# Performance work log

Measured on AMD Instinct MI355X. Metric: run time of the kernel, lower is better.

The kernel has to match this reference:

```python
import jax, jax.numpy as jnp
import numpy as np

H = 16      # headNum
C = 64      # cDim
D = 1024    # qDim = kDim = vDim = outDim
N = 2       # batch
S = 1024    # seq len


def setup_inputs() -> dict:
    key = jax.random.key(0)
    ks = jax.random.split(key, 12)
    inp = {
        "Qin": jax.random.normal(ks[0], (N, S, D), dtype=jnp.float32),
        "Kin": jax.random.normal(ks[1], (N, S, D), dtype=jnp.float32),
        "Vin": jax.random.normal(ks[2], (N, S, D), dtype=jnp.float32),
        "seqMask": jax.random.randint(ks[3], (N, S), 0, 2).astype(jnp.bool_),
        "attMask": jax.random.normal(ks[4], (1, 1, S, S), dtype=jnp.float32),
        # learned parameters (stored as [in, out] for x @ W)
        "QTrans": jax.random.normal(ks[5], (D, H * C), dtype=jnp.float32) * 0.02,
        "KTrans": jax.random.normal(ks[6], (D, H * C), dtype=jnp.float32) * 0.02,
        "VTrans": jax.random.normal(ks[7], (D, H * C), dtype=jnp.float32) * 0.02,
        "GTrans_w": jax.random.normal(ks[8], (D, H * C), dtype=jnp.float32) * 0.02,
        "GTrans_b": jnp.ones((H * C,), dtype=jnp.float32),
        "out_w": jax.random.normal(ks[9], (H * C, D), dtype=jnp.float32) * 0.02,
        "out_b": jnp.zeros((D,), dtype=jnp.float32),
    }
    return inp


def _split_heads(x):
    # [n, s, h*c] -> [h, n, s, c]
    n, s, _ = x.shape
    return x.reshape(n, s, H, C).transpose(2, 0, 1, 3)


def reference(Qin, Kin, Vin, seqMask, attMask, QTrans, KTrans, VTrans,
              GTrans_w, GTrans_b, out_w, out_b):
    Q = _split_heads(Qin @ QTrans)                         # [h,n,s,c]
    K = _split_heads(Kin @ KTrans)                         # [h,n,t,c]
    V = _split_heads(Vin @ VTrans)                         # [h,n,t,c]
    G = jax.nn.sigmoid(_split_heads(Vin @ GTrans_w + GTrans_b))  # [h,n,s,c]

    scale = 1.0 / jnp.sqrt(jnp.float32(C))
    A = jnp.einsum('hnsi,hnti->hnst', Q, K) * scale        # [h,n,s,t]
    # masked_fill where outer-product of seqMask is True
    m = (seqMask[:, :, None] & seqMask[:, None, :])[None]  # [1,n,s,t]
    A = jnp.where(m, -jnp.inf, A)
    A = A + attMask
    A = jax.nn.softmax(A, axis=-1)
    # gated attention-value reduction (eval mode: dropout inactive)
    O = jnp.einsum('hnst,hnti,hnsi->nshi', A, V, G)        # [n,s,h,c]
    O = O.reshape(O.shape[0], O.shape[1], -1)              # [n,s,h*c]
    return O @ out_w + out_b
```

## Files before the change

kernel.cpp:

```cpp
#include <hip/hip_runtime.h>
#include <hip/hip_bf16.h>
#include <cstddef>

#define S_   1024
#define HC_  1024
#define C_   64
#define LOG2E 1.4426950408889634f
#define SC2   0.18033688011112042f

typedef __attribute__((ext_vector_type(8))) short bf16x8;
typedef __attribute__((ext_vector_type(4))) short bf16x4;
typedef __attribute__((ext_vector_type(4))) float f32x4;

typedef __attribute__((address_space(1))) const void gconst_t;
typedef __attribute__((address_space(3))) void lds_t;

__device__ __forceinline__ short cvt_bf16(float f) {
  union { float f; unsigned u; } v; v.f = f;
  unsigned r = v.u + 0x7FFFu + ((v.u >> 16) & 1u);
  return (short)(r >> 16);
}
__device__ __forceinline__ float bf2f(short s) {
  union { float f; unsigned u; } v; v.u = ((unsigned)(unsigned short)s) << 16;
  return v.f;
}

template<int N> __device__ __forceinline__ void wait_vm() {
  if constexpr (N == 0)       asm volatile("s_waitcnt vmcnt(0)" ::: "memory");
  else if constexpr (N == 2)  asm volatile("s_waitcnt vmcnt(2)" ::: "memory");
  else if constexpr (N == 4)  asm volatile("s_waitcnt vmcnt(4)" ::: "memory");
  else if constexpr (N == 6)  asm volatile("s_waitcnt vmcnt(6)" ::: "memory");
  else if constexpr (N == 8)  asm volatile("s_waitcnt vmcnt(8)" ::: "memory");
  else if constexpr (N == 12) asm volatile("s_waitcnt vmcnt(12)" ::: "memory");
}

__global__ __launch_bounds__(256) void prep(
    const float* __restrict__ QT, const float* __restrict__ KT,
    const float* __restrict__ VT, const float* __restrict__ GW,
    const float* __restrict__ OW, short* __restrict__ WTb,
    const float* __restrict__ Qin, const float* __restrict__ Kin,
    const float* __restrict__ Vin, short* __restrict__ Abf,
    const float* __restrict__ att, const unsigned char* __restrict__ sm,
    short* __restrict__ biasP) {
  __shared__ short tile[32][33];
  __shared__ int a1, a4;
  const int bid = blockIdx.x;
  const int t = threadIdx.x;

  if (bid < 5120) {
    const int which = bid >> 10, xb = bid & 1023;
    const float* src = (which == 0) ? QT : (which == 1) ? KT : (which == 2) ? VT
                      : (which == 3) ? GW : OW;
    short* dst = WTb + (size_t)which * (1024u * 1024u);
    const int tj = (xb & 31) * 32;
    const int tk = (xb >> 5) * 32;
    const int r = t >> 3, c4 = (t & 7) * 4;
    const float4 v = *(const float4*)(src + (size_t)(tk + r) * 1024 + tj + c4);
    tile[c4 + 0][r] = cvt_bf16(v.x);
    tile[c4 + 1][r] = cvt_bf16(v.y);
    tile[c4 + 2][r] = cvt_bf16(v.z);
    tile[c4 + 3][r] = cvt_bf16(v.w);
    __syncthreads();
    bf16x4 o;
    o[0] = tile[r][c4 + 0]; o[1] = tile[r][c4 + 1];
    o[2] = tile[r][c4 + 2]; o[3] = tile[r][c4 + 3];
    *(bf16x4*)(dst + (size_t)(tj + r) * 1024 + tk + c4) = o;
  } else if (bid < 8192) {
    const int idx = bid - 5120;
    const int y = idx >> 10, xb = idx & 1023;
    const float* src = (y == 0) ? Qin : (y == 1) ? Kin : Vin;
    short* d = Abf + (size_t)y * 2097152u;
    const int i = (xb * 256 + t) * 8;
    const float4 a = *(const float4*)(src + i);
    const float4 b = *(const float4*)(src + i + 4);
    bf16x8 o;
    o[0] = cvt_bf16(a.x); o[1] = cvt_bf16(a.y); o[2] = cvt_bf16(a.z); o[3] = cvt_bf16(a.w);
    o[4] = cvt_bf16(b.x); o[5] = cvt_bf16(b.y); o[6] = cvt_bf16(b.z); o[7] = cvt_bf16(b.w);
    *(bf16x8*)(d + i) = o;
  } else {
    if (t == 0) { a1 = 0; a4 = 0; }
    __syncthreads();
    int l1 = 0, l4 = 0;
    for (int i = t; i < 2048; i += 256) {
      if (sm[i]) { if (i & 3) l1 = 1; else if (i & 4) l4 = 1; }
    }
    if (l1) atomicOr(&a1, 1);
    if (l4) atomicOr(&a4, 1);
    __syncthreads();
    const int mst = a1 ? 1 : (a4 ? 4 : 8);

    const int idx = bid - 8192;
    const int qw = idx & 63, tt = (idx >> 6) & 15, n = idx >> 10;
    const int lslot = t >> 2, i4 = t & 3;
    const int tc = tt * 64 + i4 * 16 + (lslot & 15);
    const int qbase = qw * 16 + ((lslot >> 4) << 2);
    const int smt = sm[(size_t)(n * 1024 + tc) * mst];
    bf16x4 o;
#pragma unroll
    for (int ii = 0; ii < 4; ii++) {
      const int q = qbase + ii;
      const int smq = sm[(size_t)(n * 1024 + q) * mst];
      const float val = (smq && smt) ? -1e4f : att[(size_t)q * 1024 + tc] * LOG2E;
      o[ii] = cvt_bf16(val);
    }
    short* dst = biasP + (((size_t)(n * 64 + qw) * 16 + tt) * 64 + lslot) * 16 + i4 * 4;
    *(bf16x4*)dst = o;
  }
}

template<int MW, int NW>
__device__ __forceinline__ void gemm_core_bf(
    const short* __restrict__ A, const short* __restrict__ BT,
    short* As, short* Bs, int m0, int n0, f32x4 acc[MW][NW]) {
  const int t = threadIdx.x;
  const int lane = t & 63, wid = t >> 6;
  const int wr = wid >> 1, wc = wid & 1;
  const int l15 = lane & 15, g = lane >> 4;
  constexpr int NT = 32;
  constexpr int LDT = MW / 2 + NW / 2;
  constexpr int ABUF = MW * 1024;
  constexpr int BBUF = NW * 1024;

#pragma unroll
  for (int m = 0; m < MW; m++)
#pragma unroll
    for (int n2 = 0; n2 < NW; n2++) acc[m][n2] = (f32x4){0.f, 0.f, 0.f, 0.f};

#define STAGE_(buf, kt)                                                        \
  {                                                                            \
    const int k0_ = (kt) * 32;                                                 \
    _Pragma("unroll")                                                          \
    for (int i_ = 0; i_ < NW / 2; i_++) {                                      \
      const int seg_ = i_ * 256 + t;                                           \
      const int row_ = seg_ >> 2, gl_ = seg_ & 3;                              \
      __builtin_amdgcn_global_load_lds(                                        \
          (gconst_t*)(BT + (size_t)(n0 + row_) * 1024 + k0_ +                  \
                      ((gl_ ^ ((row_ >> 1) & 3)) * 8)),                        \
          (lds_t*)(Bs + (buf) * BBUF + seg_ * 8), 16, 0, 0);                   \
    }                                                                          \
    _Pragma("unroll")                                                          \
    for (int i_ = 0; i_ < MW / 2; i_++) {                                      \
      const int seg_ = i_ * 256 + t;                                           \
      const int row_ = seg_ >> 2, gl_ = seg_ & 3;                              \
      __builtin_amdgcn_global_load_lds(                                        \
          (gconst_t*)(A + (size_t)(m0 + row_) * 1024 + k0_ +                   \
                      ((gl_ ^ ((row_ >> 1) & 3)) * 8)),                        \
          (lds_t*)(As + (buf) * ABUF + seg_ * 8), 16, 0, 0);                   \
    }                                                                          \
  }

  STAGE_(0, 0);
  STAGE_(1, 1);
  STAGE_(2, 2);
  int b0 = 0, b1 = 1, b2 = 2, b3 = 3;
  for (int kt = 0; kt < NT; ++kt) {
    if (kt + 2 < NT) {
      wait_vm<2 * LDT>();
    } else if (kt + 2 == NT) {
      wait_vm<LDT>();
    } else {
      wait_vm<0>();
    }
    __builtin_amdgcn_sched_barrier(0);
    __builtin_amdgcn_s_barrier();
    __builtin_amdgcn_sched_barrier(0);
    if (kt + 3 < NT) STAGE_(b3, kt + 3);

    const short* Ac = As + b0 * ABUF;
    const short* Bc = Bs + b0 * BBUF;
    bf16x8 a[MW], b[NW];
#pragma unroll
    for (int m = 0; m < MW; m++) {
      const int row = wr * (MW * 16) + m * 16 + l15;
      a[m] = *(const bf16x8*)(Ac + row * 32 + ((g ^ ((row >> 1) & 3)) * 8));
    }
#pragma unroll
    for (int n2 = 0; n2 < NW; n2++) {
      const int row = wc * (NW * 16) + n2 * 16 + l15;
      b[n2] = *(const bf16x8*)(Bc + row * 32 + ((g ^ ((row >> 1) & 3)) * 8));
    }
#pragma unroll
    for (int m = 0; m < MW; m++)
#pragma unroll
      for (int n2 = 0; n2 < NW; n2++)
        acc[m][n2] = __builtin_amdgcn_mfma_f32_16x16x32_bf16(a[m], b[n2], acc[m][n2], 0, 0, 0);
    const int tmp = b0; b0 = b1; b1 = b2; b2 = b3; b3 = tmp;
  }
#undef STAGE_
}

__global__ __launch_bounds__(256) void gemm_proj(
    const short* __restrict__ Abf, const short* __restrict__ WTb,
    short* __restrict__ Pb, short* __restrict__ VpT,
    const float* __restrict__ gb) {
  __shared__ short As[4 * 4096];
  __shared__ short Bs[4 * 4096];
  const int bid = blockIdx.x;
  const int xcd = bid & 7, ord = bid >> 3;
  const int y = xcd >> 1, nh = xcd & 1;
  const int m0 = (ord & 15) * 128;
  const int n0 = (nh * 4 + (ord >> 4)) * 128;
  const short* A = Abf + (size_t)((y <= 2) ? y : 2) * 2097152u;
  const short* BT = WTb + (size_t)y * (1024u * 1024u);
  f32x4 acc[4][4];
  gemm_core_bf<4, 4>(A, BT, As, Bs, m0, n0, acc);
  const int t = threadIdx.x, lane = t & 63, wid = t >> 6;
  const int wr = wid >> 1, wc = wid & 1, l15 = lane & 15, g = lane >> 4;

  if (y == 2) {
    short* Tr = As;
    __syncthreads();
#pragma unroll
    for (int m = 0; m < 4; m++)
#pragma unroll
      for (int n2 = 0; n2 < 4; n2++)
#pragma unroll
        for (int j = 0; j < 4; j++) {
          const int r = wr * 64 + m * 16 + g * 4 + j;
          const int c = wc * 64 + n2 * 16 + l15;
          Tr[c * 128 + r] = cvt_bf16(acc[m][n2][j]);
        }
    __syncthreads();
    const int nz = (m0 >= 1024) ? 1 : 0;
    const int sbase = m0 & 1023;
#pragma unroll
    for (int p = 0; p < 8; p++) {
      const int unit = p * 256 + t;
      const int cl = unit >> 4, sr8 = unit & 15;
      const bf16x8 v = *(const bf16x8*)(Tr + cl * 128 + sr8 * 8);
      *(bf16x8*)(VpT + ((size_t)(nz * 1024 + n0 + cl)) * 1024 + sbase + sr8 * 8) = v;
    }
  } else {
    short* outp = Pb + (size_t)y * 2097152u;
#pragma unroll
    for (int m = 0; m < 4; m++)
#pragma unroll
      for (int n2 = 0; n2 < 4; n2++)
#pragma unroll
        for (int j = 0; j < 4; j++) {
          const int row = m0 + wr * 64 + m * 16 + g * 4 + j;
          const int col = n0 + wc * 64 + n2 * 16 + l15;
          float v = acc[m][n2][j];
          if (y == 3) { v += gb[col]; v = 1.0f / (1.0f + __expf(-v)); }
          outp[(size_t)row * 1024 + col] = cvt_bf16(v);
        }
  }
}

__global__ __launch_bounds__(256) void gemm_final(
    const short* __restrict__ Aobuf, const short* __restrict__ WTo,
    float* __restrict__ outp, const float* __restrict__ ob) {
  __shared__ short As[4 * 2048];
  __shared__ short Bs[4 * 2048];
  const int bid = blockIdx.x;
  const int xcd = bid & 7, ord = bid >> 3;
  const int mg = xcd >> 1, ng = xcd & 1;
  const int m0 = (mg * 8 + (ord & 7)) * 64;
  const int n0 = (ng * 8 + (ord >> 3)) * 64;
  f32x4 acc[2][2];
  gemm_core_bf<2, 2>(Aobuf, WTo, As, Bs, m0, n0, acc);
  const int t = threadIdx.x, lane = t & 63, wid = t >> 6;
  const int wr = wid >> 1, wc = wid & 1, l15 = lane & 15, g = lane >> 4;
#pragma unroll
  for (int m = 0; m < 2; m++)
#pragma unroll
    for (int n2 = 0; n2 < 2; n2++)
#pragma unroll
      for (int j = 0; j < 4; j++) {
        const int row = m0 + wr * 32 + m * 16 + g * 4 + j;
        const int col = n0 + wc * 32 + n2 * 16 + l15;
        outp[(size_t)row * 1024 + col] = acc[m][n2][j] + ob[col];
      }
}

__global__ __launch_bounds__(256) void attn_split(
    const short* __restrict__ Qp, const short* __restrict__ Kp,
    const short* __restrict__ VpT, const short* __restrict__ biasP,
    float* __restrict__ mlbuf, short* __restrict__ OpartB, int lns) {
  __shared__ short Ks[64 * 64];
  __shared__ short Vt[64 * 64];
  __shared__ short Pl[4][16 * 64];

  const int t = threadIdx.x;
  const int lane = t & 63, w = t >> 6;
  const int l15 = lane & 15, g = lane >> 4;
  const int xb = blockIdx.x, h = blockIdx.y, n = blockIdx.z;
  const int sp = xb & ((1 << lns) - 1), qb = xb >> lns;
  const int itc = 16 >> lns;

  const int sbase = qb * 64 + w * 16;
  const short* qptr = Qp + (size_t)(n * S_ + sbase + l15) * HC_ + h * C_;
  const bf16x8 qf0 = *(const bf16x8*)(qptr + g * 8);
  const bf16x8 qf1 = *(const bf16x8*)(qptr + 32 + g * 8);

  float mrow[4], lsum[4];
  f32x4 oacc[4];
#pragma unroll
  for (int j = 0; j < 4; j++) { mrow[j] = -1e30f; lsum[j] = 0.f; }
#pragma unroll
  for (int cb = 0; cb < 4; cb++) oacc[cb] = (f32x4){0.f, 0.f, 0.f, 0.f};

  const int str = t >> 3, sc8 = (t & 7) * 8;
  const short* bbase = biasP + ((size_t)(n * 64 + qb * 4 + w) * 16 * 64 + lane) * 16;

  {
    const int t0 = sp * itc * 64;
    bf16x8 kA0 = *(const bf16x8*)(Kp + (size_t)(n * S_ + t0 + str) * HC_ + h * C_ + sc8);
    bf16x8 kA1 = *(const bf16x8*)(Kp + (size_t)(n * S_ + t0 + 32 + str) * HC_ + h * C_ + sc8);
    bf16x8 vA0 = *(const bf16x8*)(VpT + ((size_t)n * HC_ + h * C_ + str) * S_ + t0 + sc8);
    bf16x8 vA1 = *(const bf16x8*)(VpT + ((size_t)n * HC_ + h * C_ + 32 + str) * S_ + t0 + sc8);

    for (int it = 0; it < itc; ++it) {
      const int tg = sp * itc + it;
      __syncthreads();
      { const int kr = str;      *(bf16x8*)((char*)Ks + kr * 128 + ((sc8 * 2) ^ ((kr & 7) << 4))) = kA0; }
      { const int kr = 32 + str; *(bf16x8*)((char*)Ks + kr * 128 + ((sc8 * 2) ^ ((kr & 7) << 4))) = kA1; }
      { const int cr = str;      *(bf16x8*)((char*)Vt + cr * 128 + ((sc8 * 2) ^ ((cr & 7) << 4))) = vA0; }
      { const int cr = 32 + str; *(bf16x8*)((char*)Vt + cr * 128 + ((sc8 * 2) ^ ((cr & 7) << 4))) = vA1; }
      __syncthreads();

      const bf16x8 bf0 = *(const bf16x8*)(bbase + tg * 1024);
      const bf16x8 bf1 = *(const bf16x8*)(bbase + tg * 1024 + 8);
      const int t1 = ((it + 1 < itc) ? (tg + 1) : tg) * 64;
      bf16x8 kB0 = *(const bf16x8*)(Kp + (size_t)(n * S_ + t1 + str) * HC_ + h * C_ + sc8);
      bf16x8 kB1 = *(const bf16x8*)(Kp + (size_t)(n * S_ + t1 + 32 + str) * HC_ + h * C_ + sc8);
      bf16x8 vB0 = *(const bf16x8*)(VpT + ((size_t)n * HC_ + h * C_ + str) * S_ + t1 + sc8);
      bf16x8 vB1 = *(const bf16x8*)(VpT + ((size_t)n * HC_ + h * C_ + 32 + str) * S_ + t1 + sc8);

      f32x4 sacc[4];
#pragma unroll
      for (int nb = 0; nb < 4; nb++) sacc[nb] = (f32x4){0.f, 0.f, 0.f, 0.f};
      __builtin_amdgcn_s_setprio(1);
#pragma unroll
      for (int nb = 0; nb < 4; nb++) {
        const int krow = nb * 16 + l15;
        const bf16x8 b0 = *(const bf16x8*)((char*)Ks + krow * 128 + ((g * 16) ^ ((krow & 7) << 4)));
        const bf16x8 b1 = *(const bf16x8*)((char*)Ks + krow * 128 + ((64 + g * 16) ^ ((krow & 7) << 4)));
        sacc[nb] = __builtin_amdgcn_mfma_f32_16x16x32_bf16(qf0, b0, sacc[nb], 0, 0, 0);
        sacc[nb] = __builtin_amdgcn_mfma_f32_16x16x32_bf16(qf1, b1, sacc[nb], 0, 0, 0);
      }
      __builtin_amdgcn_s_setprio(0);

      float tmax[4];
#pragma unroll
      for (int j = 0; j < 4; j++) tmax[j] = -1e30f;
#pragma unroll
      for (int nb = 0; nb < 4; nb++)
#pragma unroll
        for (int j = 0; j < 4; j++) {
          const short bb = (nb < 2) ? bf0[nb * 4 + j] : bf1[(nb - 2) * 4 + j];
          const float lg = sacc[nb][j] * SC2 + bf2f(bb);
          sacc[nb][j] = lg;
          tmax[j] = fmaxf(tmax[j], lg);
        }
#pragma unroll
      for (int j = 0; j < 4; j++) {
#pragma unroll
        for (int d = 1; d < 16; d <<= 1)
          tmax[j] = fmaxf(tmax[j], __shfl_xor(tmax[j], d, 64));
        const float mn = fmaxf(mrow[j], tmax[j]);
        const float sc = exp2f(mrow[j] - mn);
        mrow[j] = mn;
        lsum[j] *= sc;
#pragma unroll
        for (int cb = 0; cb < 4; cb++) oacc[cb][j] *= sc;
        float ps = 0.f;
#pragma unroll
        for (int nb = 0; nb < 4; nb++) {
          const float p = exp2f(sacc[nb][j] - mn);
          sacc[nb][j] = p;
          ps += p;
        }
        lsum[j] += ps;
      }
      short* Pw = &Pl[w][0];
#pragma unroll
      for (int nb = 0; nb < 4; nb++)
#pragma unroll
        for (int j = 0; j < 4; j++) {
          const int pr = g * 4 + j;
          const int pcb = (nb * 16 + l15) * 2;
          *(short*)((char*)Pw + pr * 128 + (pcb ^ ((pr & 7) << 4))) = cvt_bf16(sacc[nb][j]);
        }
      __builtin_amdgcn_s_setprio(1);
#pragma unroll
      for (int kk = 0; kk < 2; kk++) {
        const bf16x8 pf = *(const bf16x8*)((char*)Pw + l15 * 128 + ((kk * 64 + g * 16) ^ ((l15 & 7) << 4)));
#pragma unroll
        for (int cb = 0; cb < 4; cb++) {
          const int vrow = cb * 16 + l15;
          const bf16x8 vf = *(const bf16x8*)((char*)Vt + vrow * 128 + ((kk * 64 + g * 16) ^ ((vrow & 7) << 4)));
          oacc[cb] = __builtin_amdgcn_mfma_f32_16x16x32_bf16(pf, vf, oacc[cb], 0, 0, 0);
        }
      }
      __builtin_amdgcn_s_setprio(0);
      kA0 = kB0; kA1 = kB1; vA0 = vB0; vA1 = vB1;
    }
  }
  const int slot = (((n * 16 + h) * 16 + qb) << lns) + sp;
  short* op = OpartB + (size_t)slot * 4096;
  float* mlp = mlbuf + (size_t)slot * 128;
#pragma unroll
  for (int j = 0; j < 4; j++) {
    float rs = lsum[j];
#pragma unroll
    for (int d = 1; d < 16; d <<= 1) rs += __shfl_xor(rs, d, 64);
    const int row = w * 16 + g * 4 + j;
#pragma unroll
    for (int cb = 0; cb < 4; cb++)
      op[row * 64 + cb * 16 + l15] = cvt_bf16(oacc[cb][j]);
    if (l15 == 0) { mlp[row * 2] = mrow[j]; mlp[row * 2 + 1] = rs; }
  }
}

__global__ __launch_bounds__(256) void attn_merge(
    const short* __restrict__ OpartB, const float* __restrict__ mlbuf,
    const short* __restrict__ Gp, short* __restrict__ ObufB, int lns) {
  const int qb = blockIdx.x, h = blockIdx.y, n = blockIdx.z;
  const int nsplit = 1 << lns;
  const int t = threadIdx.x;
  const int r = t >> 2, c0 = (t & 3) * 16;
  const int bslot = ((n * 16 + h) * 16 + qb) << lns;
  const float* mlb = mlbuf + (size_t)bslot * 128 + r * 2;

  float M = -1e30f;
  for (int sp = 0; sp < nsplit; sp++) M = fmaxf(M, mlb[(size_t)sp * 128]);
  float l = 0.f;
  for (int sp = 0; sp < nsplit; sp++)
    l += exp2f(mlb[(size_t)sp * 128] - M) * mlb[(size_t)sp * 128 + 1];
  const float inv = 1.0f / l;

  float acc[16];
#pragma unroll
  for (int k = 0; k < 16; k++) acc[k] = 0.f;
  for (int sp = 0; sp < nsplit; sp++) {
    const float wsc = exp2f(mlb[(size_t)sp * 128] - M);
    const short* op = OpartB + (size_t)(bslot + sp) * 4096 + r * 64 + c0;
    const bf16x8 v0 = *(const bf16x8*)(op);
    const bf16x8 v1 = *(const bf16x8*)(op + 8);
#pragma unroll
    for (int k = 0; k < 8; k++) {
      acc[k]     += wsc * bf2f(v0[k]);
      acc[8 + k] += wsc * bf2f(v1[k]);
    }
  }
  const int srow = qb * 64 + r;
  const size_t idx = (size_t)(n * S_ + srow) * HC_ + h * C_ + c0;
  const bf16x8 g0 = *(const bf16x8*)(Gp + idx);
  const bf16x8 g1 = *(const bf16x8*)(Gp + idx + 8);
  bf16x8 o0, o1;
#pragma unroll
  for (int k = 0; k < 8; k++) {
    o0[k] = cvt_bf16(acc[k] * inv * bf2f(g0[k]));
    o1[k] = cvt_bf16(acc[8 + k] * inv * bf2f(g1[k]));
  }
  *(bf16x8*)(ObufB + idx) = o0;
  *(bf16x8*)(ObufB + idx + 8) = o1;
}

extern "C" void kernel_launch(void* const* d_in, const int* in_sizes, int n_in,
                              void* d_out, int out_size, void* d_ws, size_t ws_size,
                              hipStream_t stream) {
  const float* Qin      = (const float*)d_in[0];
  const float* Kin      = (const float*)d_in[1];
  const float* Vin      = (const float*)d_in[2];
  const void*  seqMask  = d_in[3];
  const float* attMask  = (const float*)d_in[4];
  const float* QTrans   = (const float*)d_in[5];
  const float* KTrans   = (const float*)d_in[6];
  const float* VTrans   = (const float*)d_in[7];
  const float* GTrans_w = (const float*)d_in[8];
  const float* GTrans_b = (const float*)d_in[9];
  const float* out_w    = (const float*)d_in[10];
  const float* out_b    = (const float*)d_in[11];
  float* out = (float*)d_out;

  char* ws = (char*)d_ws;
  const size_t MB = 1048576u;
  short* WTb   = (short*)(ws);
  short* Abf   = (short*)(ws + 10 * MB);
  short* Pb    = (short*)(ws + 22 * MB);
  short* VpT   = (short*)(ws + 38 * MB);
  short* ObufB = (short*)(ws + 42 * MB);
  short* biasP = (short*)(ws + 46 * MB);
  const size_t partBase = 51 * MB;

  const short* Kp = Pb + (size_t)1u * 2097152u;
  const short* Gp = Pb + (size_t)3u * 2097152u;

  int lns = 0;
  for (int c = 1; c >= 0; c--) {
    const size_t slots = 512u << c;
    if (ws_size >= partBase + slots * (8192u + 512u)) { lns = c; break; }
  }
  const size_t slots = 512u << lns;
  short* OpartB = (short*)(ws + partBase);
  float* mlbuf  = (float*)(ws + partBase + slots * 8192u);

  hipLaunchKernelGGL(prep, dim3(10240), dim3(256), 0, stream,
                     QTrans, KTrans, VTrans, GTrans_w, out_w, WTb,
                     Qin, Kin, Vin, Abf,
                     attMask, (const unsigned char*)seqMask, biasP);
  hipLaunchKernelGGL(gemm_proj, dim3(512), dim3(256), 0, stream,
                     Abf, WTb, Pb, VpT, GTrans_b);
  hipLaunchKernelGGL(attn_split, dim3(16 << lns, 16, 2), dim3(256), 0, stream,
                     Pb, Kp, VpT, biasP, mlbuf, OpartB, lns);
  hipLaunchKernelGGL(attn_merge, dim3(16, 16, 2), dim3(256), 0, stream,
                     OpartB, mlbuf, Gp, ObufB, lns);
  hipLaunchKernelGGL(gemm_final, dim3(512), dim3(256), 0, stream,
                     ObufB, WTb + (size_t)4u * 1048576u, out, out_b);
}
```

Before: 112.1 us.

## Fuse split-attention merge and gating into the output projection GEMM

Removes the attn_merge kernel and folds its work into gemm_final. The GEMM computes per-row split weights from the m/l buffers in LDS, then builds each A tile on the fly by combining the two partial outputs, normalizing, and multiplying by the gate. This drops one launch and the write and read of the intermediate O buffer. The cost is that each N-column block recomputes the merge, and the A tile loads become synchronous register loads instead of async LDS loads. The code also handles at most two splits.

```diff
diff --git a/kernel.cpp b/kernel.cpp
--- a/kernel.cpp
+++ b/kernel.cpp
@@ -248,19 +248,109 @@
 }
 
 __global__ __launch_bounds__(256) void gemm_final(
-    const short* __restrict__ Aobuf, const short* __restrict__ WTo,
-    float* __restrict__ outp, const float* __restrict__ ob) {
-  __shared__ short As[4 * 2048];
-  __shared__ short Bs[4 * 2048];
+    const short* __restrict__ OpartB, const float* __restrict__ mlbuf,
+    const short* __restrict__ Gp, const short* __restrict__ WTo,
+    float* __restrict__ outp, const float* __restrict__ ob, int lns) {
+  __shared__ short As[2 * 2048];
+  __shared__ short Bs[2 * 2048];
+  __shared__ float wscf[16][64][2];
   const int bid = blockIdx.x;
   const int xcd = bid & 7, ord = bid >> 3;
   const int mg = xcd >> 1, ng = xcd & 1;
   const int m0 = (mg * 8 + (ord & 7)) * 64;
   const int n0 = (ng * 8 + (ord >> 3)) * 64;
+  const int t = threadIdx.x;
+  const int lane = t & 63, wid = t >> 6;
+  const int wr = wid >> 1, wc = wid & 1;
+  const int l15 = lane & 15, g = lane >> 4;
+  const int nsplit = 1 << lns;
+  const int nn = m0 >> 10, s0 = m0 & 1023, qb = (m0 >> 6) & 15;
+
+  for (int u = t; u < 16 * 64; u += 256) {
+    const int h = u >> 6, row = u & 63;
+    const int bslot = ((nn * 16 + h) * 16 + qb) << lns;
+    const float* mlb = mlbuf + (size_t)bslot * 128 + row * 2;
+    float M = -1e30f;
+    for (int sp = 0; sp < nsplit; sp++) M = fmaxf(M, mlb[(size_t)sp * 128]);
+    float l = 0.f;
+    for (int sp = 0; sp < nsplit; sp++)
+      l += exp2f(mlb[(size_t)sp * 128] - M) * mlb[(size_t)sp * 128 + 1];
+    const float inv = 1.0f / l;
+    wscf[h][row][0] = exp2f(mlb[0] - M) * inv;
+    wscf[h][row][1] = (nsplit > 1) ? exp2f(mlb[128] - M) * inv : 0.f;
+  }
+  __syncthreads();
+
+  const int arow = t >> 2, ac8 = (t & 3) * 8;
+  const int brow = t >> 2, bgl = t & 3;
+
+#define BUILD_A_(buf, kt)                                                      \
+  {                                                                            \
+    const int h_ = (kt) >> 1, hf_ = (kt) & 1;                                  \
+    const int slotb_ = ((nn * 16 + h_) * 16 + qb) << lns;                      \
+    const short* p0_ = OpartB + (size_t)slotb_ * 4096 + arow * 64 + hf_ * 32 + ac8; \
+    const bf16x8 q0_ = *(const bf16x8*)p0_;                                    \
+    const bf16x8 q1_ = (nsplit > 1) ? *(const bf16x8*)(p0_ + 4096) : q0_;      \
+    const float w0_ = wscf[h_][arow][0];                                       \
+    const float w1_ = wscf[h_][arow][1];                                       \
+    const bf16x8 gt_ = *(const bf16x8*)(Gp + ((size_t)(nn * 1024 + s0 + arow)) * 1024 + h_ * 64 + hf_ * 32 + ac8); \
+    bf16x8 o_;                                                                 \
+    _Pragma("unroll")                                                          \
+    for (int j_ = 0; j_ < 8; j_++) {                                           \
+      const float a_ = (w0_ * bf2f(q0_[j_]) + w1_ * bf2f(q1_[j_])) * bf2f(gt_[j_]); \
+      o_[j_] = cvt_bf16(a_);                                                   \
+    }                                                                          \
+    *(bf16x8*)(As + (buf) * 2048 + arow * 32 + (((ac8 >> 3) ^ ((arow >> 1) & 3)) * 8)) = o_; \
+  }
+
+#define STAGE_B_(buf, kt)                                                      \
+  {                                                                            \
+    const int k0_ = (kt) * 32;                                                 \
+    __builtin_amdgcn_global_load_lds(                                          \
+        (gconst_t*)(WTo + (size_t)(n0 + brow) * 1024 + k0_ +                   \
+                    ((bgl ^ ((brow >> 1) & 3)) * 8)),                          \
+        (lds_t*)(Bs + (buf) * 2048 + t * 8), 16, 0, 0);                        \
+  }
+
   f32x4 acc[2][2];
-  gemm_core_bf<2, 2>(Aobuf, WTo, As, Bs, m0, n0, acc);
-  const int t = threadIdx.x, lane = t & 63, wid = t >> 6;
-  const int wr = wid >> 1, wc = wid & 1, l15 = lane & 15, g = lane >> 4;
+#pragma unroll
+  for (int m = 0; m < 2; m++)
+#pragma unroll
+    for (int n2 = 0; n2 < 2; n2++) acc[m][n2] = (f32x4){0.f, 0.f, 0.f, 0.f};
+
+  STAGE_B_(0, 0);
+  BUILD_A_(0, 0);
+  __syncthreads();
+
+  for (int kt = 0; kt < 32; ++kt) {
+    const int pb = kt & 1;
+    const short* Ac = As + pb * 2048;
+    const short* Bc = Bs + pb * 2048;
+    bf16x8 a[2], b[2];
+#pragma unroll
+    for (int m = 0; m < 2; m++) {
+      const int row = wr * 32 + m * 16 + l15;
+      a[m] = *(const bf16x8*)(Ac + row * 32 + ((g ^ ((row >> 1) & 3)) * 8));
+    }
+#pragma unroll
+    for (int n2 = 0; n2 < 2; n2++) {
+      const int row = wc * 32 + n2 * 16 + l15;
+      b[n2] = *(const bf16x8*)(Bc + row * 32 + ((g ^ ((row >> 1) & 3)) * 8));
+    }
+    if (kt + 1 < 32) {
+      STAGE_B_(pb ^ 1, kt + 1);
+      BUILD_A_(pb ^ 1, kt + 1);
+    }
+#pragma unroll
+    for (int m = 0; m < 2; m++)
+#pragma unroll
+      for (int n2 = 0; n2 < 2; n2++)
+        acc[m][n2] = __builtin_amdgcn_mfma_f32_16x16x32_bf16(a[m], b[n2], acc[m][n2], 0, 0, 0);
+    __syncthreads();
+  }
+#undef BUILD_A_
+#undef STAGE_B_
+
 #pragma unroll
   for (int m = 0; m < 2; m++)
 #pragma unroll
@@ -411,51 +501,6 @@
       op[row * 64 + cb * 16 + l15] = cvt_bf16(oacc[cb][j]);
     if (l15 == 0) { mlp[row * 2] = mrow[j]; mlp[row * 2 + 1] = rs; }
   }
-}
-
-__global__ __launch_bounds__(256) void attn_merge(
-    const short* __restrict__ OpartB, const float* __restrict__ mlbuf,
-    const short* __restrict__ Gp, short* __restrict__ ObufB, int lns) {
-  const int qb = blockIdx.x, h = blockIdx.y, n = blockIdx.z;
-  const int nsplit = 1 << lns;
-  const int t = threadIdx.x;
-  const int r = t >> 2, c0 = (t & 3) * 16;
-  const int bslot = ((n * 16 + h) * 16 + qb) << lns;
-  const float* mlb = mlbuf + (size_t)bslot * 128 + r * 2;
-
-  float M = -1e30f;
-  for (int sp = 0; sp < nsplit; sp++) M = fmaxf(M, mlb[(size_t)sp * 128]);
-  float l = 0.f;
-  for (int sp = 0; sp < nsplit; sp++)
-    l += exp2f(mlb[(size_t)sp * 128] - M) * mlb[(size_t)sp * 128 + 1];
-  const float inv = 1.0f / l;
-
-  float acc[16];
-#pragma unroll
-  for (int k = 0; k < 16; k++) acc[k] = 0.f;
-  for (int sp = 0; sp < nsplit; sp++) {
-    const float wsc = exp2f(mlb[(size_t)sp * 128] - M);
-    const short* op = OpartB + (size_t)(bslot + sp) * 4096 + r * 64 + c0;
-    const bf16x8 v0 = *(const bf16x8*)(op);
-    const bf16x8 v1 = *(const bf16x8*)(op + 8);
-#pragma unroll
-    for (int k = 0; k < 8; k++) {
-      acc[k]     += wsc * bf2f(v0[k]);
-      acc[8 + k] += wsc * bf2f(v1[k]);
-    }
-  }
-  const int srow = qb * 64 + r;
-  const size_t idx = (size_t)(n * S_ + srow) * HC_ + h * C_ + c0;
-  const bf16x8 g0 = *(const bf16x8*)(Gp + idx);
-  const bf16x8 g1 = *(const bf16x8*)(Gp + idx + 8);
-  bf16x8 o0, o1;
-#pragma unroll
-  for (int k = 0; k < 8; k++) {
-    o0[k] = cvt_bf16(acc[k] * inv * bf2f(g0[k]));
-    o1[k] = cvt_bf16(acc[8 + k] * inv * bf2f(g1[k]));
-  }
-  *(bf16x8*)(ObufB + idx) = o0;
-  *(bf16x8*)(ObufB + idx + 8) = o1;
 }
 
 extern "C" void kernel_launch(void* const* d_in, const int* in_sizes, int n_in,
@@ -481,7 +526,6 @@
   short* Abf   = (short*)(ws + 10 * MB);
   short* Pb    = (short*)(ws + 22 * MB);
   short* VpT   = (short*)(ws + 38 * MB);
-  short* ObufB = (short*)(ws + 42 * MB);
   short* biasP = (short*)(ws + 46 * MB);
   const size_t partBase = 51 * MB;
 
@@ -505,8 +549,7 @@
                      Abf, WTb, Pb, VpT, GTrans_b);
   hipLaunchKernelGGL(attn_split, dim3(16 << lns, 16, 2), dim3(256), 0, stream,
                      Pb, Kp, VpT, biasP, mlbuf, OpartB, lns);
-  hipLaunchKernelGGL(attn_merge, dim3(16, 16, 2), dim3(256), 0, stream,
-                     OpartB, mlbuf, Gp, ObufB, lns);
   hipLaunchKernelGGL(gemm_final, dim3(512), dim3(256), 0, stream,
-                     ObufB, WTb + (size_t)4u * 1048576u, out, out_b);
-}
+                     OpartB, mlbuf, Gp, WTb + (size_t)4u * 1048576u,
+                     out, out_b, lns);
+}
```

Result: slower. 120.0 us (+7.0%).

## Switch GEMM core to double-buffered BK=64 pipeline with setprio around MFMAs

Applied to the files above, without the earlier changes.

Replaces the four-stage BK=32 LDS ring, which used explicit vmcnt waits and a barrier per step, with a two-stage BK=64 double buffer. The new loop does 16 iterations with two MFMA k-steps each, a wider XOR swizzle, and __syncthreads once per iteration. It raises wave priority around the MFMA block. This halves the number of barriers, but leaves only one stage of prefetch to hide load latency. The __syncthreads that relies on __syncthreads() after the final iteration before the LDS transpose is removed.

```diff
diff --git a/kernel.cpp b/kernel.cpp
--- a/kernel.cpp
+++ b/kernel.cpp
@@ -23,15 +23,6 @@
 __device__ __forceinline__ float bf2f(short s) {
   union { float f; unsigned u; } v; v.u = ((unsigned)(unsigned short)s) << 16;
   return v.f;
-}
-
-template<int N> __device__ __forceinline__ void wait_vm() {
-  if constexpr (N == 0)       asm volatile("s_waitcnt vmcnt(0)" ::: "memory");
-  else if constexpr (N == 2)  asm volatile("s_waitcnt vmcnt(2)" ::: "memory");
-  else if constexpr (N == 4)  asm volatile("s_waitcnt vmcnt(4)" ::: "memory");
-  else if constexpr (N == 6)  asm volatile("s_waitcnt vmcnt(6)" ::: "memory");
-  else if constexpr (N == 8)  asm volatile("s_waitcnt vmcnt(8)" ::: "memory");
-  else if constexpr (N == 12) asm volatile("s_waitcnt vmcnt(12)" ::: "memory");
 }
 
 __global__ __launch_bounds__(256) void prep(
@@ -116,10 +107,8 @@
   const int lane = t & 63, wid = t >> 6;
   const int wr = wid >> 1, wc = wid & 1;
   const int l15 = lane & 15, g = lane >> 4;
-  constexpr int NT = 32;
-  constexpr int LDT = MW / 2 + NW / 2;
-  constexpr int ABUF = MW * 1024;
-  constexpr int BBUF = NW * 1024;
+  constexpr int ABUF = MW * 2048;
+  constexpr int BBUF = NW * 2048;
 
 #pragma unroll
   for (int m = 0; m < MW; m++)
@@ -128,63 +117,60 @@
 
 #define STAGE_(buf, kt)                                                        \
   {                                                                            \
-    const int k0_ = (kt) * 32;                                                 \
+    const int k0_ = (kt) * 64;                                                 \
     _Pragma("unroll")                                                          \
-    for (int i_ = 0; i_ < NW / 2; i_++) {                                      \
+    for (int i_ = 0; i_ < NW; i_++) {                                          \
       const int seg_ = i_ * 256 + t;                                           \
-      const int row_ = seg_ >> 2, gl_ = seg_ & 3;                              \
+      const int row_ = seg_ >> 3, gl_ = seg_ & 7;                              \
       __builtin_amdgcn_global_load_lds(                                        \
           (gconst_t*)(BT + (size_t)(n0 + row_) * 1024 + k0_ +                  \
-                      ((gl_ ^ ((row_ >> 1) & 3)) * 8)),                        \
+                      ((gl_ ^ (row_ & 7)) * 8)),                               \
           (lds_t*)(Bs + (buf) * BBUF + seg_ * 8), 16, 0, 0);                   \
     }                                                                          \
     _Pragma("unroll")                                                          \
-    for (int i_ = 0; i_ < MW / 2; i_++) {                                      \
+    for (int i_ = 0; i_ < MW; i_++) {                                          \
       const int seg_ = i_ * 256 + t;                                           \
-      const int row_ = seg_ >> 2, gl_ = seg_ & 3;                              \
+      const int row_ = seg_ >> 3, gl_ = seg_ & 7;                              \
       __builtin_amdgcn_global_load_lds(                                        \
           (gconst_t*)(A + (size_t)(m0 + row_) * 1024 + k0_ +                   \
-                      ((gl_ ^ ((row_ >> 1) & 3)) * 8)),                        \
+                      ((gl_ ^ (row_ & 7)) * 8)),                               \
           (lds_t*)(As + (buf) * ABUF + seg_ * 8), 16, 0, 0);                   \
     }                                                                          \
   }
 
   STAGE_(0, 0);
-  STAGE_(1, 1);
-  STAGE_(2, 2);
-  int b0 = 0, b1 = 1, b2 = 2, b3 = 3;
-  for (int kt = 0; kt < NT; ++kt) {
-    if (kt + 2 < NT) {
-      wait_vm<2 * LDT>();
-    } else if (kt + 2 == NT) {
-      wait_vm<LDT>();
-    } else {
-      wait_vm<0>();
-    }
-    __builtin_amdgcn_sched_barrier(0);
-    __builtin_amdgcn_s_barrier();
-    __builtin_amdgcn_sched_barrier(0);
-    if (kt + 3 < NT) STAGE_(b3, kt + 3);
-
-    const short* Ac = As + b0 * ABUF;
-    const short* Bc = Bs + b0 * BBUF;
-    bf16x8 a[MW], b[NW];
+  __syncthreads();
+  int cur = 0;
+  for (int kt = 0; kt < 16; ++kt) {
+    if (kt + 1 < 16) STAGE_(cur ^ 1, kt + 1);
+    const short* Ac = As + cur * ABUF;
+    const short* Bc = Bs + cur * BBUF;
+    bf16x8 a[MW][2], b[NW][2];
 #pragma unroll
     for (int m = 0; m < MW; m++) {
       const int row = wr * (MW * 16) + m * 16 + l15;
-      a[m] = *(const bf16x8*)(Ac + row * 32 + ((g ^ ((row >> 1) & 3)) * 8));
+#pragma unroll
+      for (int kk = 0; kk < 2; kk++)
+        a[m][kk] = *(const bf16x8*)(Ac + row * 64 + (((kk * 4 + g) ^ (row & 7)) * 8));
     }
 #pragma unroll
     for (int n2 = 0; n2 < NW; n2++) {
       const int row = wc * (NW * 16) + n2 * 16 + l15;
-      b[n2] = *(const bf16x8*)(Bc + row * 32 + ((g ^ ((row >> 1) & 3)) * 8));
-    }
-#pragma unroll
-    for (int m = 0; m < MW; m++)
-#pragma unroll
-      for (int n2 = 0; n2 < NW; n2++)
-        acc[m][n2] = __builtin_amdgcn_mfma_f32_16x16x32_bf16(a[m], b[n2], acc[m][n2], 0, 0, 0);
-    const int tmp = b0; b0 = b1; b1 = b2; b2 = b3; b3 = tmp;
+#pragma unroll
+      for (int kk = 0; kk < 2; kk++)
+        b[n2][kk] = *(const bf16x8*)(Bc + row * 64 + (((kk * 4 + g) ^ (row & 7)) * 8));
+    }
+    __builtin_amdgcn_s_setprio(1);
+#pragma unroll
+    for (int kk = 0; kk < 2; kk++)
+#pragma unroll
+      for (int m = 0; m < MW; m++)
+#pragma unroll
+        for (int n2 = 0; n2 < NW; n2++)
+          acc[m][n2] = __builtin_amdgcn_mfma_f32_16x16x32_bf16(a[m][kk], b[n2][kk], acc[m][n2], 0, 0, 0);
+    __builtin_amdgcn_s_setprio(0);
+    __syncthreads();
+    cur ^= 1;
   }
 #undef STAGE_
 }
@@ -193,8 +179,8 @@
     const short* __restrict__ Abf, const short* __restrict__ WTb,
     short* __restrict__ Pb, short* __restrict__ VpT,
     const float* __restrict__ gb) {
-  __shared__ short As[4 * 4096];
-  __shared__ short Bs[4 * 4096];
+  __shared__ short As[2 * 8192];
+  __shared__ short Bs[2 * 8192];
   const int bid = blockIdx.x;
   const int xcd = bid & 7, ord = bid >> 3;
   const int y = xcd >> 1, nh = xcd & 1;
@@ -209,7 +195,6 @@
 
   if (y == 2) {
     short* Tr = As;
-    __syncthreads();
 #pragma unroll
     for (int m = 0; m < 4; m++)
 #pragma unroll
@@ -250,8 +235,8 @@
 __global__ __launch_bounds__(256) void gemm_final(
     const short* __restrict__ Aobuf, const short* __restrict__ WTo,
     float* __restrict__ outp, const float* __restrict__ ob) {
-  __shared__ short As[4 * 2048];
-  __shared__ short Bs[4 * 2048];
+  __shared__ short As[2 * 4096];
+  __shared__ short Bs[2 * 4096];
   const int bid = blockIdx.x;
   const int xcd = bid & 7, ord = bid >> 3;
   const int mg = xcd >> 1, ng = xcd & 1;
```

Result: faster. 103.2 us (median of 2 runs) (-8.0%).
